# Kernel optimization log

Hardware: AMD Instinct MI355X
Metric: run time of the kernel (lower is better)

Reference implementation:

```python
import jax, jax.numpy as jnp
import numpy as np

BLOCK = 8
ITERS = 8
EPS = 1e-5
SHAPE = (64, 64, 64)
BATCH = 16


def overlapping_blocks(x, bs):
    # x: [B, M, N, K] -> per-block copies with a 1-cell zero-padded halo:
    # [B, nm, nn, nk, bs+2, bs+2, bs+2]
    B, M, N, K = x.shape
    p = jnp.pad(x, ((0, 0), (1, 1), (1, 1), (1, 1)))

    def gather(a, axis, n, size):
        idx = (jnp.arange(n)[:, None] * bs + jnp.arange(size)[None, :]).reshape(-1)
        a = jnp.take(a, idx, axis=axis)
        return a.reshape(a.shape[:axis] + (n, size) + a.shape[axis + 1:])

    nm, nn, nk = M // bs, N // bs, K // bs
    p = gather(p, 1, nm, bs + 2)   # [B, nm, P, N+2, K+2]
    p = gather(p, 3, nn, bs + 2)   # [B, nm, P, nn, P, K+2]
    p = gather(p, 5, nk, bs + 2)   # [B, nm, P, nn, P, nk, P]
    return p.transpose(0, 1, 3, 5, 2, 4, 6)


def param_blocks(w, bs):
    # [..., M, N, K] -> [..., nm, nn, nk, bs, bs, bs] (non-overlapping)
    lead = w.shape[:-3]
    M, N, K = w.shape[-3:]
    w = w.reshape(*lead, M // bs, bs, N // bs, bs, K // bs, bs)
    nl = len(lead)
    perm = tuple(range(nl)) + (nl, nl + 2, nl + 4, nl + 1, nl + 3, nl + 5)
    return w.transpose(perm)


def gridnet_step(weight, bias, residual_scale, x, inner_iterations, block_size,
                 eps=EPS, normalize=True):
    bs = block_size
    blocks = overlapping_blocks(x, bs)            # [B, nm, nn, nk, P, P, P]
    wb = param_blocks(weight, bs)                 # [27, nm, nn, nk, bs, bs, bs]
    bb = param_blocks(bias, bs)                   # [nm, nn, nk, bs, bs, bs]
    rb = param_blocks(residual_scale, bs)
    inner = (slice(None),) * 4 + (slice(1, -1),) * 3

    for _ in range(inner_iterations):
        if normalize:
            mean = blocks.mean(axis=(-3, -2, -1), keepdims=True)
            var = blocks.var(axis=(-3, -2, -1), keepdims=True)
            normed = (blocks - mean) / jnp.sqrt(var + eps)
        else:
            normed = blocks
        dot = jnp.zeros_like(blocks[inner])
        tap = 0
        for dx in range(3):
            for dy in range(3):
                for dz in range(3):
                    nb = normed[..., dx:dx + bs, dy:dy + bs, dz:dz + bs]
                    dot = dot + nb * wb[tap]
                    tap += 1
        out = blocks[inner] + rb * jax.nn.silu(dot + bb)
        # only interior cells update; halo stays at initial (synced) values
        blocks = blocks.at[inner].set(out)

    y = blocks[inner]                              # [B, nm, nn, nk, bs, bs, bs]
    B, nm, nn, nk = y.shape[:4]
    return y.transpose(0, 1, 4, 2, 5, 3, 6).reshape(B, nm * bs, nn * bs, nk * bs)


def setup_inputs() -> dict:
    key = jax.random.key(0)
    k_w, k_x = jax.random.split(key)
    M, N, K = SHAPE
    weight = jax.random.normal(k_w, (27, M, N, K), dtype=jnp.float32) / np.sqrt(27.0).astype(np.float32)
    bias = jnp.zeros((M, N, K), dtype=jnp.float32)
    residual_scale = jnp.ones((M, N, K), dtype=jnp.float32)
    x = jax.random.normal(k_x, (BATCH, M, N, K), dtype=jnp.float32)
    return {"weight": weight, "bias": bias, "residual_scale": residual_scale, "x": x}


def reference(weight, bias, residual_scale, x):
    return gridnet_step(weight, bias, residual_scale, x, ITERS, BLOCK, EPS, True)
```

## Files before the change

### kernel.cpp

```cpp
#include <hip/hip_runtime.h>

typedef _Float16 h2 __attribute__((ext_vector_type(2)));

#define COLH 10

template <int CTRL>
__device__ __forceinline__ float dpp_stage(float v) {
    int x = __builtin_amdgcn_update_dpp(0, __float_as_int(v), CTRL, 0xf, 0xf, true);
    return v + __int_as_float(x);
}
__device__ __forceinline__ float wave_sum(float v) {
    v = dpp_stage<0x111>(v);
    v = dpp_stage<0x112>(v);
    v = dpp_stage<0x114>(v);
    v = dpp_stage<0x118>(v);
    v = dpp_stage<0x142>(v);
    v = dpp_stage<0x143>(v);
    return v;
}

#define RFL(x) __int_as_float(__builtin_amdgcn_readfirstlane(__float_as_int(x)))

__device__ __forceinline__ h2 mid2(h2 lo, h2 hi) {
    int r = __builtin_amdgcn_alignbit(__builtin_bit_cast(int, hi),
                                      __builtin_bit_cast(int, lo), 16);
    return __builtin_bit_cast(h2, r);
}

#define R27(M) M(0) M(1) M(2) M(3) M(4) M(5) M(6) M(7) M(8) M(9) M(10) M(11) \
    M(12) M(13) M(14) M(15) M(16) M(17) M(18) M(19) M(20) M(21) M(22) M(23)  \
    M(24) M(25) M(26)

#define LOADW(T) float2 f##T = *(const float2*)(W + ((size_t)(T) << 18) + ofs); \
                 h2 w##T = { (_Float16)f##T.x, (_Float16)f##T.y };              \
                 sw0 += (float)w##T.x; sw1 += (float)w##T.y;

#define LINE(BP, DD, L, WA, WB, WC) {                                         \
    const h2 v0 = BP[(((L) / 3) * 10 + (L) % 3) * 5];                         \
    const h2 v1 = BP[(((L) / 3) * 10 + (L) % 3) * 5 + 1];                     \
    const h2 vm = mid2(v0, v1);                                               \
    DD = __builtin_elementwise_fma(v0, WA, DD);                               \
    DD = __builtin_elementwise_fma(vm, WB, DD);                               \
    DD = __builtin_elementwise_fma(v1, WC, DD);  }

#define DOT9(BP, DD)                                                          \
    LINE(BP, DD, 0, w0,  w1,  w2)                                             \
    LINE(BP, DD, 1, w3,  w4,  w5)                                             \
    LINE(BP, DD, 2, w6,  w7,  w8)                                             \
    LINE(BP, DD, 3, w9,  w10, w11)                                            \
    LINE(BP, DD, 4, w12, w13, w14)                                            \
    LINE(BP, DD, 5, w15, w16, w17)                                            \
    LINE(BP, DD, 6, w18, w19, w20)                                            \
    LINE(BP, DD, 7, w21, w22, w23)                                            \
    LINE(BP, DD, 8, w24, w25, w26)

#define EPI(SFX, DST) {                                                       \
    float mean = (halo_s##SFX + Si##SFX) * inv_n;                             \
    float istd = rsqrtf((halo_q##SFX + Qi##SFX) * inv_n - mean*mean + 1e-5f); \
    float u0 = ((float)dd##SFX.x - mean * sw0) * istd + bias0;                \
    float u1 = ((float)dd##SFX.y - mean * sw1) * istd + bias1;                \
    c0##SFX += rs0 * (u0 * __builtin_amdgcn_rcpf(1.f + __expf(-u0)));         \
    c1##SFX += rs1 * (u1 * __builtin_amdgcn_rcpf(1.f + __expf(-u1)));         \
    DST[ipc]     = (_Float16)c0##SFX;                                         \
    DST[ipc + 1] = (_Float16)c1##SFX;  }

#define ITERPAIR(SA, DA, SB, DB, RED) {                                       \
    const h2* bpA = (const h2*)&SA[base_h];                                   \
    const h2* bpB = (const h2*)&SB[base_h];                                   \
    h2 ddA = { (_Float16)0.f, (_Float16)0.f };                                \
    h2 ddB = ddA;                                                             \
    DOT9(bpA, ddA)                                                            \
    DOT9(bpB, ddB)                                                            \
    EPI(A, DA)                                                                \
    EPI(B, DB)                                                                \
    float spA = wave_sum(c0A + c1A);                                          \
    float qpA = wave_sum(c0A * c0A + c1A * c1A);                              \
    float spB = wave_sum(c0B + c1B);                                          \
    float qpB = wave_sum(c0B * c0B + c1B * c1B);                              \
    if (lane == 63) { RED[0][wave] = make_float2(spA, qpA);                   \
                      RED[1][wave] = make_float2(spB, qpB); }                 \
    __syncthreads();                                                          \
    SiA = RFL(RED[0][0].x + RED[0][1].x + RED[0][2].x + RED[0][3].x);         \
    QiA = RFL(RED[0][0].y + RED[0][1].y + RED[0][2].y + RED[0][3].y);         \
    SiB = RFL(RED[1][0].x + RED[1][1].x + RED[1][2].x + RED[1][3].x);         \
    QiB = RFL(RED[1][0].y + RED[1][1].y + RED[1][2].y + RED[1][3].y); }

__global__ __launch_bounds__(256)
void gridnet_kernel(const float* __restrict__ W,
                    const float* __restrict__ Bias,
                    const float* __restrict__ Rs,
                    const float* __restrict__ X,
                    float* __restrict__ Y,
                    int n_batch)
{
    __shared__ __align__(16) _Float16 bufA0[100 * COLH];
    __shared__ __align__(16) _Float16 bufA1[100 * COLH];
    __shared__ __align__(16) _Float16 bufB0[100 * COLH];
    __shared__ __align__(16) _Float16 bufB1[100 * COLH];
    __shared__ float4 red4[8];
    __shared__ float2 redP[2][2][4];

    const int tid  = threadIdx.x;
    const int h    = tid & 3;
    const int ly   = (tid >> 2) & 7;
    const int lx   = tid >> 5;
    const int wave = tid >> 6;
    const int lane = tid & 63;

    const int np    = n_batch >> 1;
    const int bid   = blockIdx.x;
    const int r     = bid / np;
    const int pb    = bid - r * np;
    const int batch = 2 * pb;
    const int gm0 = (r >> 6) << 3;
    const int gn0 = ((r >> 3) & 7) << 3;
    const int gk0 = (r & 7) << 3;

    const float* xbA = X + ((size_t)batch << 18);

    float sA_all = 0.f, qA_all = 0.f, sA_int = 0.f, qA_int = 0.f;
    float sB_all = 0.f, qB_all = 0.f, sB_int = 0.f, qB_int = 0.f;
    for (int i = tid; i < 1000; i += 256) {
        int ix = i / 100;
        int rem = i - ix * 100;
        int iy = rem / 10;
        int iz = rem - iy * 10;
        int m = gm0 + ix - 1, n = gn0 + iy - 1, k = gk0 + iz - 1;
        float vA = 0.f, vB = 0.f;
        if ((unsigned)m < 64u && (unsigned)n < 64u && (unsigned)k < 64u) {
            const float* p = xbA + (m << 12) + (n << 6) + k;
            vA = p[0];
            vB = p[1 << 18];
        }
        _Float16 hvA = (_Float16)vA;
        _Float16 hvB = (_Float16)vB;
        int a = (ix * 10 + iy) * COLH + iz;
        bufA0[a] = hvA; bufA1[a] = hvA;
        bufB0[a] = hvB; bufB1[a] = hvB;
        float fA = (float)hvA, fB = (float)hvB;
        sA_all += fA; qA_all += fA * fA;
        sB_all += fB; qB_all += fB * fB;
        bool interior = ((unsigned)(ix - 1) < 8u) & ((unsigned)(iy - 1) < 8u) &
                        ((unsigned)(iz - 1) < 8u);
        if (interior) { sA_int += fA; qA_int += fA * fA;
                        sB_int += fB; qB_int += fB * fB; }
    }

    const int gm = gm0 + lx, gn = gn0 + ly, gk = gk0 + 2 * h;
    const size_t ofs = ((size_t)gm << 12) + (gn << 6) + gk;

    float sw0 = 0.f, sw1 = 0.f;
    R27(LOADW)
    const float2 bf = *(const float2*)(Bias + ofs);
    const float2 rf = *(const float2*)(Rs + ofs);
    const float bias0 = bf.x, bias1 = bf.y;
    const float rs0 = rf.x, rs1 = rf.y;

    __syncthreads();

    const int base_h = (lx * 10 + ly) * COLH + 2 * h;
    const int ipc    = ((lx + 1) * 10 + (ly + 1)) * COLH + (2 * h + 1);
    float c0A = (float)bufA0[ipc];
    float c1A = (float)bufA0[ipc + 1];
    float c0B = (float)bufB0[ipc];
    float c1B = (float)bufB0[ipc + 1];

    {
        float a0 = wave_sum(sA_all);
        float a1 = wave_sum(qA_all);
        float a2 = wave_sum(sA_int);
        float a3 = wave_sum(qA_int);
        float b0 = wave_sum(sB_all);
        float b1 = wave_sum(qB_all);
        float b2 = wave_sum(sB_int);
        float b3 = wave_sum(qB_int);
        if (lane == 63) {
            red4[wave]     = make_float4(a0, a1, a2, a3);
            red4[4 + wave] = make_float4(b0, b1, b2, b3);
        }
    }
    __syncthreads();
    float SA_all = 0.f, QA_all = 0.f, SiA = 0.f, QiA = 0.f;
    float SB_all = 0.f, QB_all = 0.f, SiB = 0.f, QiB = 0.f;
    #pragma unroll
    for (int wv = 0; wv < 4; ++wv) {
        float4 tA = red4[wv];
        float4 tB = red4[4 + wv];
        SA_all += tA.x; QA_all += tA.y; SiA += tA.z; QiA += tA.w;
        SB_all += tB.x; QB_all += tB.y; SiB += tB.z; QiB += tB.w;
    }
    const float halo_sA = RFL(SA_all - SiA);
    const float halo_qA = RFL(QA_all - QiA);
    const float halo_sB = RFL(SB_all - SiB);
    const float halo_qB = RFL(QB_all - QiB);
    SiA = RFL(SiA); QiA = RFL(QiA);
    SiB = RFL(SiB); QiB = RFL(QiB);

    const float inv_n = 1.0f / 1000.0f;

    #pragma unroll 1
    for (int it = 0; it < 4; ++it) {
        ITERPAIR(bufA0, bufA1, bufB0, bufB1, redP[0])
        ITERPAIR(bufA1, bufA0, bufB1, bufB0, redP[1])
    }

    float* yp = Y + ((size_t)batch << 18) + ofs;
    *(float2*)(yp)             = make_float2(c0A, c1A);
    *(float2*)(yp + (1 << 18)) = make_float2(c0B, c1B);
}

extern "C" void kernel_launch(void* const* d_in, const int* in_sizes, int n_in,
                              void* d_out, int out_size, void* d_ws, size_t ws_size,
                              hipStream_t stream) {
    const float* W = (const float*)d_in[0];
    const float* B = (const float*)d_in[1];
    const float* R = (const float*)d_in[2];
    const float* X = (const float*)d_in[3];
    float* Y = (float*)d_out;

    int n_batch = in_sizes[3] >> 18;
    dim3 grid(512 * (n_batch >> 1)), block(256);
    hipLaunchKernelGGL(gridnet_kernel, grid, block, 0, stream, W, B, R, X, Y, n_batch);
}
```

Baseline: 154.2 us.

## Process four batch samples per block to amortize weight loads

Each workgroup now handles four batch elements instead of two, halving the grid. The 27-tap weights, bias and residual scales loaded per thread are reused across twice as many samples, and the four independent stencil chains give more instruction-level parallelism within each iteration. The initial statistics reduction is moved ahead of the weight load so one barrier covers both it and the LDS fill. In exchange it uses more registers and twice the LDS per block, and there are fewer blocks to hide latency.

```diff
diff --git a/kernel.cpp b/kernel.cpp
--- a/kernel.cpp
+++ b/kernel.cpp
@@ -64,26 +64,42 @@
     DST[ipc]     = (_Float16)c0##SFX;                                         \
     DST[ipc + 1] = (_Float16)c1##SFX;  }
 
-#define ITERPAIR(SA, DA, SB, DB, RED) {                                       \
+#define ITER4(SA, DA, SB, DB, SC, DC, SD, DDst, RED) {                        \
     const h2* bpA = (const h2*)&SA[base_h];                                   \
     const h2* bpB = (const h2*)&SB[base_h];                                   \
+    const h2* bpC = (const h2*)&SC[base_h];                                   \
+    const h2* bpD = (const h2*)&SD[base_h];                                   \
     h2 ddA = { (_Float16)0.f, (_Float16)0.f };                                \
-    h2 ddB = ddA;                                                             \
+    h2 ddB = ddA, ddC = ddA, ddD = ddA;                                       \
     DOT9(bpA, ddA)                                                            \
     DOT9(bpB, ddB)                                                            \
+    DOT9(bpC, ddC)                                                            \
+    DOT9(bpD, ddD)                                                            \
     EPI(A, DA)                                                                \
     EPI(B, DB)                                                                \
+    EPI(C, DC)                                                                \
+    EPI(D, DDst)                                                              \
     float spA = wave_sum(c0A + c1A);                                          \
     float qpA = wave_sum(c0A * c0A + c1A * c1A);                              \
     float spB = wave_sum(c0B + c1B);                                          \
     float qpB = wave_sum(c0B * c0B + c1B * c1B);                              \
+    float spC = wave_sum(c0C + c1C);                                          \
+    float qpC = wave_sum(c0C * c0C + c1C * c1C);                              \
+    float spD = wave_sum(c0D + c1D);                                          \
+    float qpD = wave_sum(c0D * c0D + c1D * c1D);                              \
     if (lane == 63) { RED[0][wave] = make_float2(spA, qpA);                   \
-                      RED[1][wave] = make_float2(spB, qpB); }                 \
+                      RED[1][wave] = make_float2(spB, qpB);                   \
+                      RED[2][wave] = make_float2(spC, qpC);                   \
+                      RED[3][wave] = make_float2(spD, qpD); }                 \
     __syncthreads();                                                          \
     SiA = RFL(RED[0][0].x + RED[0][1].x + RED[0][2].x + RED[0][3].x);         \
     QiA = RFL(RED[0][0].y + RED[0][1].y + RED[0][2].y + RED[0][3].y);         \
     SiB = RFL(RED[1][0].x + RED[1][1].x + RED[1][2].x + RED[1][3].x);         \
-    QiB = RFL(RED[1][0].y + RED[1][1].y + RED[1][2].y + RED[1][3].y); }
+    QiB = RFL(RED[1][0].y + RED[1][1].y + RED[1][2].y + RED[1][3].y);         \
+    SiC = RFL(RED[2][0].x + RED[2][1].x + RED[2][2].x + RED[2][3].x);         \
+    QiC = RFL(RED[2][0].y + RED[2][1].y + RED[2][2].y + RED[2][3].y);         \
+    SiD = RFL(RED[3][0].x + RED[3][1].x + RED[3][2].x + RED[3][3].x);         \
+    QiD = RFL(RED[3][0].y + RED[3][1].y + RED[3][2].y + RED[3][3].y); }
 
 __global__ __launch_bounds__(256)
 void gridnet_kernel(const float* __restrict__ W,
@@ -97,8 +113,12 @@
     __shared__ __align__(16) _Float16 bufA1[100 * COLH];
     __shared__ __align__(16) _Float16 bufB0[100 * COLH];
     __shared__ __align__(16) _Float16 bufB1[100 * COLH];
-    __shared__ float4 red4[8];
-    __shared__ float2 redP[2][2][4];
+    __shared__ __align__(16) _Float16 bufC0[100 * COLH];
+    __shared__ __align__(16) _Float16 bufC1[100 * COLH];
+    __shared__ __align__(16) _Float16 bufD0[100 * COLH];
+    __shared__ __align__(16) _Float16 bufD1[100 * COLH];
+    __shared__ float4 red4[4][4];
+    __shared__ float2 redP[2][4][4];
 
     const int tid  = threadIdx.x;
     const int h    = tid & 3;
@@ -107,11 +127,11 @@
     const int wave = tid >> 6;
     const int lane = tid & 63;
 
-    const int np    = n_batch >> 1;
+    const int np    = n_batch >> 2;
     const int bid   = blockIdx.x;
     const int r     = bid / np;
     const int pb    = bid - r * np;
-    const int batch = 2 * pb;
+    const int batch = 4 * pb;
     const int gm0 = (r >> 6) << 3;
     const int gn0 = ((r >> 3) & 7) << 3;
     const int gk0 = (r & 7) << 3;
@@ -120,30 +140,57 @@
 
     float sA_all = 0.f, qA_all = 0.f, sA_int = 0.f, qA_int = 0.f;
     float sB_all = 0.f, qB_all = 0.f, sB_int = 0.f, qB_int = 0.f;
+    float sC_all = 0.f, qC_all = 0.f, sC_int = 0.f, qC_int = 0.f;
+    float sD_all = 0.f, qD_all = 0.f, sD_int = 0.f, qD_int = 0.f;
     for (int i = tid; i < 1000; i += 256) {
         int ix = i / 100;
         int rem = i - ix * 100;
         int iy = rem / 10;
         int iz = rem - iy * 10;
         int m = gm0 + ix - 1, n = gn0 + iy - 1, k = gk0 + iz - 1;
-        float vA = 0.f, vB = 0.f;
+        float vA = 0.f, vB = 0.f, vC = 0.f, vD = 0.f;
         if ((unsigned)m < 64u && (unsigned)n < 64u && (unsigned)k < 64u) {
             const float* p = xbA + (m << 12) + (n << 6) + k;
             vA = p[0];
             vB = p[1 << 18];
+            vC = p[2 << 18];
+            vD = p[3 << 18];
         }
-        _Float16 hvA = (_Float16)vA;
-        _Float16 hvB = (_Float16)vB;
+        _Float16 hvA = (_Float16)vA, hvB = (_Float16)vB;
+        _Float16 hvC = (_Float16)vC, hvD = (_Float16)vD;
         int a = (ix * 10 + iy) * COLH + iz;
         bufA0[a] = hvA; bufA1[a] = hvA;
         bufB0[a] = hvB; bufB1[a] = hvB;
-        float fA = (float)hvA, fB = (float)hvB;
+        bufC0[a] = hvC; bufC1[a] = hvC;
+        bufD0[a] = hvD; bufD1[a] = hvD;
+        float fA = (float)hvA, fB = (float)hvB, fC = (float)hvC, fD = (float)hvD;
         sA_all += fA; qA_all += fA * fA;
         sB_all += fB; qB_all += fB * fB;
+        sC_all += fC; qC_all += fC * fC;
+        sD_all += fD; qD_all += fD * fD;
         bool interior = ((unsigned)(ix - 1) < 8u) & ((unsigned)(iy - 1) < 8u) &
                         ((unsigned)(iz - 1) < 8u);
         if (interior) { sA_int += fA; qA_int += fA * fA;
-                        sB_int += fB; qB_int += fB * fB; }
+                        sB_int += fB; qB_int += fB * fB;
+                        sC_int += fC; qC_int += fC * fC;
+                        sD_int += fD; qD_int += fD * fD; }
+    }
+
+    {
+        float a0 = wave_sum(sA_all), a1 = wave_sum(qA_all);
+        float a2 = wave_sum(sA_int), a3 = wave_sum(qA_int);
+        float b0 = wave_sum(sB_all), b1 = wave_sum(qB_all);
+        float b2 = wave_sum(sB_int), b3 = wave_sum(qB_int);
+        float c0 = wave_sum(sC_all), c1 = wave_sum(qC_all);
+        float c2 = wave_sum(sC_int), c3 = wave_sum(qC_int);
+        float d0 = wave_sum(sD_all), d1 = wave_sum(qD_all);
+        float d2 = wave_sum(sD_int), d3 = wave_sum(qD_int);
+        if (lane == 63) {
+            red4[0][wave] = make_float4(a0, a1, a2, a3);
+            red4[1][wave] = make_float4(b0, b1, b2, b3);
+            red4[2][wave] = make_float4(c0, c1, c2, c3);
+            red4[3][wave] = make_float4(d0, d1, d2, d3);
+        }
     }
 
     const int gm = gm0 + lx, gn = gn0 + ly, gk = gk0 + 2 * h;
@@ -160,53 +207,48 @@
 
     const int base_h = (lx * 10 + ly) * COLH + 2 * h;
     const int ipc    = ((lx + 1) * 10 + (ly + 1)) * COLH + (2 * h + 1);
-    float c0A = (float)bufA0[ipc];
-    float c1A = (float)bufA0[ipc + 1];
-    float c0B = (float)bufB0[ipc];
-    float c1B = (float)bufB0[ipc + 1];
-
-    {
-        float a0 = wave_sum(sA_all);
-        float a1 = wave_sum(qA_all);
-        float a2 = wave_sum(sA_int);
-        float a3 = wave_sum(qA_int);
-        float b0 = wave_sum(sB_all);
-        float b1 = wave_sum(qB_all);
-        float b2 = wave_sum(sB_int);
-        float b3 = wave_sum(qB_int);
-        if (lane == 63) {
-            red4[wave]     = make_float4(a0, a1, a2, a3);
-            red4[4 + wave] = make_float4(b0, b1, b2, b3);
-        }
-    }
-    __syncthreads();
+    float c0A = (float)bufA0[ipc], c1A = (float)bufA0[ipc + 1];
+    float c0B = (float)bufB0[ipc], c1B = (float)bufB0[ipc + 1];
+    float c0C = (float)bufC0[ipc], c1C = (float)bufC0[ipc + 1];
+    float c0D = (float)bufD0[ipc], c1D = (float)bufD0[ipc + 1];
+
     float SA_all = 0.f, QA_all = 0.f, SiA = 0.f, QiA = 0.f;
     float SB_all = 0.f, QB_all = 0.f, SiB = 0.f, QiB = 0.f;
+    float SC_all = 0.f, QC_all = 0.f, SiC = 0.f, QiC = 0.f;
+    float SD_all = 0.f, QD_all = 0.f, SiD = 0.f, QiD = 0.f;
     #pragma unroll
     for (int wv = 0; wv < 4; ++wv) {
-        float4 tA = red4[wv];
-        float4 tB = red4[4 + wv];
+        float4 tA = red4[0][wv];
+        float4 tB = red4[1][wv];
+        float4 tC = red4[2][wv];
+        float4 tD = red4[3][wv];
         SA_all += tA.x; QA_all += tA.y; SiA += tA.z; QiA += tA.w;
         SB_all += tB.x; QB_all += tB.y; SiB += tB.z; QiB += tB.w;
-    }
-    const float halo_sA = RFL(SA_all - SiA);
-    const float halo_qA = RFL(QA_all - QiA);
-    const float halo_sB = RFL(SB_all - SiB);
-    const float halo_qB = RFL(QB_all - QiB);
+        SC_all += tC.x; QC_all += tC.y; SiC += tC.z; QiC += tC.w;
+        SD_all += tD.x; QD_all += tD.y; SiD += tD.z; QiD += tD.w;
+    }
+    const float halo_sA = RFL(SA_all - SiA), halo_qA = RFL(QA_all - QiA);
+    const float halo_sB = RFL(SB_all - SiB), halo_qB = RFL(QB_all - QiB);
+    const float halo_sC = RFL(SC_all - SiC), halo_qC = RFL(QC_all - QiC);
+    const float halo_sD = RFL(SD_all - SiD), halo_qD = RFL(QD_all - QiD);
     SiA = RFL(SiA); QiA = RFL(QiA);
     SiB = RFL(SiB); QiB = RFL(QiB);
+    SiC = RFL(SiC); QiC = RFL(QiC);
+    SiD = RFL(SiD); QiD = RFL(QiD);
 
     const float inv_n = 1.0f / 1000.0f;
 
     #pragma unroll 1
     for (int it = 0; it < 4; ++it) {
-        ITERPAIR(bufA0, bufA1, bufB0, bufB1, redP[0])
-        ITERPAIR(bufA1, bufA0, bufB1, bufB0, redP[1])
+        ITER4(bufA0, bufA1, bufB0, bufB1, bufC0, bufC1, bufD0, bufD1, redP[0])
+        ITER4(bufA1, bufA0, bufB1, bufB0, bufC1, bufC0, bufD1, bufD0, redP[1])
     }
 
     float* yp = Y + ((size_t)batch << 18) + ofs;
     *(float2*)(yp)             = make_float2(c0A, c1A);
     *(float2*)(yp + (1 << 18)) = make_float2(c0B, c1B);
+    *(float2*)(yp + (2 << 18)) = make_float2(c0C, c1C);
+    *(float2*)(yp + (3 << 18)) = make_float2(c0D, c1D);
 }
 
 extern "C" void kernel_launch(void* const* d_in, const int* in_sizes, int n_in,
@@ -219,6 +261,6 @@
     float* Y = (float*)d_out;
 
     int n_batch = in_sizes[3] >> 18;
-    dim3 grid(512 * (n_batch >> 1)), block(256);
+    dim3 grid(512 * (n_batch >> 2)), block(256);
     hipLaunchKernelGGL(gridnet_kernel, grid, block, 0, stream, W, B, R, X, Y, n_batch);
 }
```

Result: no change. 153.8 us (-0.2%).

## Split block halves across two batches, four outputs per thread

Applied to the files above, without the earlier changes.

Work is remapped so each half of the 256-thread block handles one of the two batch elements, and each thread computes four consecutive k-outputs instead of two outputs for each of two batches. Weights are loaded as float4 and converted with packed RTZ conversion, and the shared-memory row pitch grows from 10 to 14 halves so each thread's 3-word column window stays aligned. The per-iteration reduction now covers two waves per batch. The aim is to reuse loaded stencil rows across more outputs and cut redundant mid2 and load work, in exchange for more registers and changed LDS access patterns.

```diff
diff --git a/kernel.cpp b/kernel.cpp
--- a/kernel.cpp
+++ b/kernel.cpp
@@ -2,7 +2,8 @@
 
 typedef _Float16 h2 __attribute__((ext_vector_type(2)));
 
-#define COLH 10
+#define CSTR 7
+#define COLH 14
 
 template <int CTRL>
 __device__ __forceinline__ float dpp_stage(float v) {
@@ -26,64 +27,63 @@
                                       __builtin_bit_cast(int, lo), 16);
     return __builtin_bit_cast(h2, r);
 }
+__device__ __forceinline__ h2 pkrtz(float a, float b) {
+    return __builtin_bit_cast(h2, __builtin_amdgcn_cvt_pkrtz(a, b));
+}
 
 #define R27(M) M(0) M(1) M(2) M(3) M(4) M(5) M(6) M(7) M(8) M(9) M(10) M(11) \
     M(12) M(13) M(14) M(15) M(16) M(17) M(18) M(19) M(20) M(21) M(22) M(23)  \
     M(24) M(25) M(26)
 
-#define LOADW(T) float2 f##T = *(const float2*)(W + ((size_t)(T) << 18) + ofs); \
-                 h2 w##T = { (_Float16)f##T.x, (_Float16)f##T.y };              \
-                 sw0 += (float)w##T.x; sw1 += (float)w##T.y;
-
-#define LINE(BP, DD, L, WA, WB, WC) {                                         \
-    const h2 v0 = BP[(((L) / 3) * 10 + (L) % 3) * 5];                         \
-    const h2 v1 = BP[(((L) / 3) * 10 + (L) % 3) * 5 + 1];                     \
-    const h2 vm = mid2(v0, v1);                                               \
-    DD = __builtin_elementwise_fma(v0, WA, DD);                               \
-    DD = __builtin_elementwise_fma(vm, WB, DD);                               \
-    DD = __builtin_elementwise_fma(v1, WC, DD);  }
-
-#define DOT9(BP, DD)                                                          \
-    LINE(BP, DD, 0, w0,  w1,  w2)                                             \
-    LINE(BP, DD, 1, w3,  w4,  w5)                                             \
-    LINE(BP, DD, 2, w6,  w7,  w8)                                             \
-    LINE(BP, DD, 3, w9,  w10, w11)                                            \
-    LINE(BP, DD, 4, w12, w13, w14)                                            \
-    LINE(BP, DD, 5, w15, w16, w17)                                            \
-    LINE(BP, DD, 6, w18, w19, w20)                                            \
-    LINE(BP, DD, 7, w21, w22, w23)                                            \
-    LINE(BP, DD, 8, w24, w25, w26)
-
-#define EPI(SFX, DST) {                                                       \
-    float mean = (halo_s##SFX + Si##SFX) * inv_n;                             \
-    float istd = rsqrtf((halo_q##SFX + Qi##SFX) * inv_n - mean*mean + 1e-5f); \
-    float u0 = ((float)dd##SFX.x - mean * sw0) * istd + bias0;                \
-    float u1 = ((float)dd##SFX.y - mean * sw1) * istd + bias1;                \
-    c0##SFX += rs0 * (u0 * __builtin_amdgcn_rcpf(1.f + __expf(-u0)));         \
-    c1##SFX += rs1 * (u1 * __builtin_amdgcn_rcpf(1.f + __expf(-u1)));         \
-    DST[ipc]     = (_Float16)c0##SFX;                                         \
-    DST[ipc + 1] = (_Float16)c1##SFX;  }
-
-#define ITERPAIR(SA, DA, SB, DB, RED) {                                       \
-    const h2* bpA = (const h2*)&SA[base_h];                                   \
-    const h2* bpB = (const h2*)&SB[base_h];                                   \
-    h2 ddA = { (_Float16)0.f, (_Float16)0.f };                                \
-    h2 ddB = ddA;                                                             \
-    DOT9(bpA, ddA)                                                            \
-    DOT9(bpB, ddB)                                                            \
-    EPI(A, DA)                                                                \
-    EPI(B, DB)                                                                \
-    float spA = wave_sum(c0A + c1A);                                          \
-    float qpA = wave_sum(c0A * c0A + c1A * c1A);                              \
-    float spB = wave_sum(c0B + c1B);                                          \
-    float qpB = wave_sum(c0B * c0B + c1B * c1B);                              \
-    if (lane == 63) { RED[0][wave] = make_float2(spA, qpA);                   \
-                      RED[1][wave] = make_float2(spB, qpB); }                 \
-    __syncthreads();                                                          \
-    SiA = RFL(RED[0][0].x + RED[0][1].x + RED[0][2].x + RED[0][3].x);         \
-    QiA = RFL(RED[0][0].y + RED[0][1].y + RED[0][2].y + RED[0][3].y);         \
-    SiB = RFL(RED[1][0].x + RED[1][1].x + RED[1][2].x + RED[1][3].x);         \
-    QiB = RFL(RED[1][0].y + RED[1][1].y + RED[1][2].y + RED[1][3].y); }
+#define LOADW(T)                                                               \
+    float4 f##T = *(const float4*)(W + ((size_t)(T) << 18) + ofs);             \
+    h2 w##T##p = pkrtz(f##T.x, f##T.y);                                        \
+    h2 w##T##q = pkrtz(f##T.z, f##T.w);                                        \
+    sw0 += f##T.x; sw1 += f##T.y; sw2 += f##T.z; sw3 += f##T.w;
+
+#define COLN(BP, O, T0, T1, T2) {                                              \
+    h2 d0 = BP[(O)], d1 = BP[(O) + 1], d2 = BP[(O) + 2];                       \
+    h2 m0 = mid2(d0, d1), m1 = mid2(d1, d2);                                   \
+    dd0 = __builtin_elementwise_fma(d0, w##T0##p, dd0);                        \
+    dd1 = __builtin_elementwise_fma(d1, w##T0##q, dd1);                        \
+    dd0 = __builtin_elementwise_fma(m0, w##T1##p, dd0);                        \
+    dd1 = __builtin_elementwise_fma(m1, w##T1##q, dd1);                        \
+    dd0 = __builtin_elementwise_fma(d1, w##T2##p, dd0);                        \
+    dd1 = __builtin_elementwise_fma(d2, w##T2##q, dd1); }
+
+#define SILU(U) ((U) * __builtin_amdgcn_rcpf(1.f + __expf(-(U))))
+
+#define ITERX(BP, DSTB, RED) {                                                 \
+    h2 dd0 = { (_Float16)0.f, (_Float16)0.f };                                 \
+    h2 dd1 = dd0;                                                              \
+    COLN(BP, 0,    0,  1,  2)                                                  \
+    COLN(BP, 7,    3,  4,  5)                                                  \
+    COLN(BP, 14,   6,  7,  8)                                                  \
+    COLN(BP, 70,   9, 10, 11)                                                  \
+    COLN(BP, 77,  12, 13, 14)                                                  \
+    COLN(BP, 84,  15, 16, 17)                                                  \
+    COLN(BP, 140, 18, 19, 20)                                                  \
+    COLN(BP, 147, 21, 22, 23)                                                  \
+    COLN(BP, 154, 24, 25, 26)                                                  \
+    float mean = (halo_s + Si) * inv_n;                                        \
+    float istd = rsqrtf((halo_q + Qi) * inv_n - mean * mean + 1e-5f);          \
+    float u0 = ((float)dd0.x - mean * sw0) * istd + bf.x;                      \
+    float u1 = ((float)dd0.y - mean * sw1) * istd + bf.y;                      \
+    float u2 = ((float)dd1.x - mean * sw2) * istd + bf.z;                      \
+    float u3 = ((float)dd1.y - mean * sw3) * istd + bf.w;                      \
+    c0 += rf.x * SILU(u0);                                                     \
+    c1 += rf.y * SILU(u1);                                                     \
+    c2 += rf.z * SILU(u2);                                                     \
+    c3 += rf.w * SILU(u3);                                                     \
+    DSTB[ipc] = (_Float16)c0;                                                  \
+    *(h2*)&DSTB[ipc + 1] = pkrtz(c1, c2);                                      \
+    DSTB[ipc + 3] = (_Float16)c3;                                              \
+    float sp = wave_sum((c0 + c1) + (c2 + c3));                                \
+    float qp = wave_sum((c0 * c0 + c1 * c1) + (c2 * c2 + c3 * c3));            \
+    if (lane == 63) RED[bh][wv1] = make_float2(sp, qp);                        \
+    __syncthreads();                                                           \
+    Si = RFL(RED[bh][0].x + RED[bh][1].x);                                     \
+    Qi = RFL(RED[bh][0].y + RED[bh][1].y); }
 
 __global__ __launch_bounds__(256)
 void gridnet_kernel(const float* __restrict__ W,
@@ -97,26 +97,28 @@
     __shared__ __align__(16) _Float16 bufA1[100 * COLH];
     __shared__ __align__(16) _Float16 bufB0[100 * COLH];
     __shared__ __align__(16) _Float16 bufB1[100 * COLH];
-    __shared__ float4 red4[8];
-    __shared__ float2 redP[2][2][4];
-
-    const int tid  = threadIdx.x;
-    const int h    = tid & 3;
-    const int ly   = (tid >> 2) & 7;
-    const int lx   = tid >> 5;
+    __shared__ float4 red4[2][4];
+    __shared__ float2 redP[2][2][2];
+
+    const int tid = threadIdx.x;
+    const int h    = tid & 1;
+    const int ly   = (tid >> 1) & 7;
+    const int lx   = (tid >> 4) & 7;
+    const int bh   = tid >> 7;
     const int wave = tid >> 6;
     const int lane = tid & 63;
+    const int wv1  = wave & 1;
 
     const int np    = n_batch >> 1;
     const int bid   = blockIdx.x;
     const int r     = bid / np;
     const int pb    = bid - r * np;
-    const int batch = 2 * pb;
+    const int batch2 = 2 * pb;
     const int gm0 = (r >> 6) << 3;
     const int gn0 = ((r >> 3) & 7) << 3;
     const int gk0 = (r & 7) << 3;
 
-    const float* xbA = X + ((size_t)batch << 18);
+    const float* xb = X + ((size_t)batch2 << 18);
 
     float sA_all = 0.f, qA_all = 0.f, sA_int = 0.f, qA_int = 0.f;
     float sB_all = 0.f, qB_all = 0.f, sB_int = 0.f, qB_int = 0.f;
@@ -128,16 +130,15 @@
         int m = gm0 + ix - 1, n = gn0 + iy - 1, k = gk0 + iz - 1;
         float vA = 0.f, vB = 0.f;
         if ((unsigned)m < 64u && (unsigned)n < 64u && (unsigned)k < 64u) {
-            const float* p = xbA + (m << 12) + (n << 6) + k;
+            const float* p = xb + (m << 12) + (n << 6) + k;
             vA = p[0];
             vB = p[1 << 18];
         }
-        _Float16 hvA = (_Float16)vA;
-        _Float16 hvB = (_Float16)vB;
+        _Float16 hA = (_Float16)vA, hB = (_Float16)vB;
         int a = (ix * 10 + iy) * COLH + iz;
-        bufA0[a] = hvA; bufA1[a] = hvA;
-        bufB0[a] = hvB; bufB1[a] = hvB;
-        float fA = (float)hvA, fB = (float)hvB;
+        bufA0[a] = hA; bufA1[a] = hA;
+        bufB0[a] = hB; bufB1[a] = hB;
+        float fA = (float)hA, fB = (float)hB;
         sA_all += fA; qA_all += fA * fA;
         sB_all += fB; qB_all += fB * fB;
         bool interior = ((unsigned)(ix - 1) < 8u) & ((unsigned)(iy - 1) < 8u) &
@@ -146,67 +147,54 @@
                         sB_int += fB; qB_int += fB * fB; }
     }
 
-    const int gm = gm0 + lx, gn = gn0 + ly, gk = gk0 + 2 * h;
-    const size_t ofs = ((size_t)gm << 12) + (gn << 6) + gk;
-
-    float sw0 = 0.f, sw1 = 0.f;
+    const int gm = gm0 + lx, gn = gn0 + ly;
+    const size_t ofs = ((size_t)gm << 12) + (gn << 6) + gk0 + 4 * h;
+    float sw0 = 0.f, sw1 = 0.f, sw2 = 0.f, sw3 = 0.f;
     R27(LOADW)
-    const float2 bf = *(const float2*)(Bias + ofs);
-    const float2 rf = *(const float2*)(Rs + ofs);
-    const float bias0 = bf.x, bias1 = bf.y;
-    const float rs0 = rf.x, rs1 = rf.y;
-
+    const float4 bf = *(const float4*)(Bias + ofs);
+    const float4 rf = *(const float4*)(Rs + ofs);
+
+    {
+        float a0 = wave_sum(sA_all), a1 = wave_sum(qA_all);
+        float a2 = wave_sum(sA_int), a3 = wave_sum(qA_int);
+        float b0 = wave_sum(sB_all), b1 = wave_sum(qB_all);
+        float b2 = wave_sum(sB_int), b3 = wave_sum(qB_int);
+        if (lane == 63) {
+            red4[0][wave] = make_float4(a0, a1, a2, a3);
+            red4[1][wave] = make_float4(b0, b1, b2, b3);
+        }
+    }
     __syncthreads();
 
-    const int base_h = (lx * 10 + ly) * COLH + 2 * h;
-    const int ipc    = ((lx + 1) * 10 + (ly + 1)) * COLH + (2 * h + 1);
-    float c0A = (float)bufA0[ipc];
-    float c1A = (float)bufA0[ipc + 1];
-    float c0B = (float)bufB0[ipc];
-    float c1B = (float)bufB0[ipc + 1];
-
-    {
-        float a0 = wave_sum(sA_all);
-        float a1 = wave_sum(qA_all);
-        float a2 = wave_sum(sA_int);
-        float a3 = wave_sum(qA_int);
-        float b0 = wave_sum(sB_all);
-        float b1 = wave_sum(qB_all);
-        float b2 = wave_sum(sB_int);
-        float b3 = wave_sum(qB_int);
-        if (lane == 63) {
-            red4[wave]     = make_float4(a0, a1, a2, a3);
-            red4[4 + wave] = make_float4(b0, b1, b2, b3);
-        }
-    }
-    __syncthreads();
-    float SA_all = 0.f, QA_all = 0.f, SiA = 0.f, QiA = 0.f;
-    float SB_all = 0.f, QB_all = 0.f, SiB = 0.f, QiB = 0.f;
+    float S_all = 0.f, Q_all = 0.f, Si = 0.f, Qi = 0.f;
     #pragma unroll
     for (int wv = 0; wv < 4; ++wv) {
-        float4 tA = red4[wv];
-        float4 tB = red4[4 + wv];
-        SA_all += tA.x; QA_all += tA.y; SiA += tA.z; QiA += tA.w;
-        SB_all += tB.x; QB_all += tB.y; SiB += tB.z; QiB += tB.w;
-    }
-    const float halo_sA = RFL(SA_all - SiA);
-    const float halo_qA = RFL(QA_all - QiA);
-    const float halo_sB = RFL(SB_all - SiB);
-    const float halo_qB = RFL(QB_all - QiB);
-    SiA = RFL(SiA); QiA = RFL(QiA);
-    SiB = RFL(SiB); QiB = RFL(QiB);
+        float4 t = red4[bh][wv];
+        S_all += t.x; Q_all += t.y; Si += t.z; Qi += t.w;
+    }
+    const float halo_s = RFL(S_all - Si);
+    const float halo_q = RFL(Q_all - Qi);
+    Si = RFL(Si); Qi = RFL(Qi);
+
+    _Float16* const my0 = bh ? bufB0 : bufA0;
+    _Float16* const my1 = bh ? bufB1 : bufA1;
+    const int bpD = (lx * 10 + ly) * CSTR + 2 * h;
+    const h2* const bp0 = (const h2*)my0 + bpD;
+    const h2* const bp1 = (const h2*)my1 + bpD;
+    const int ipc = ((lx + 1) * 10 + (ly + 1)) * COLH + 4 * h + 1;
+    float c0 = (float)my0[ipc],     c1 = (float)my0[ipc + 1];
+    float c2 = (float)my0[ipc + 2], c3 = (float)my0[ipc + 3];
 
     const float inv_n = 1.0f / 1000.0f;
 
     #pragma unroll 1
     for (int it = 0; it < 4; ++it) {
-        ITERPAIR(bufA0, bufA1, bufB0, bufB1, redP[0])
-        ITERPAIR(bufA1, bufA0, bufB1, bufB0, redP[1])
-    }
-
-    float* yp = Y + ((size_t)batch << 18) + ofs;
-    *(float2*)(yp)             = make_float2(c0A, c1A);
-    *(float2*)(yp + (1 << 18)) = make_float2(c0B, c1B);
+        ITERX(bp0, my1, redP[0])
+        ITERX(bp1, my0, redP[1])
+    }
+
+    float* yp = Y + ((size_t)(batch2 + bh) << 18) + ofs;
+    *(float4*)yp = make_float4(c0, c1, c2, c3);
 }
 
 extern "C" void kernel_launch(void* const* d_in, const int* in_sizes, int n_in,
```

After: 167.7 us. +8.8%, slower.
